# Kernel tuning notes

Hardware: AMD Instinct MI355X
Metric: run time of the kernel (lower is better)

Reference implementation:

```python
import jax, jax.numpy as jnp
import numpy as np
import math

B, NQ, NK = 8, 1024, 2048
DQ = DK = DV = 1024
H = 8
DH = DV // H
EPS = 1e-5


def _layernorm(x, g, b):
    mu = jnp.mean(x, axis=-1, keepdims=True)
    var = jnp.mean(jnp.square(x - mu), axis=-1, keepdims=True)
    return (x - mu) * jax.lax.rsqrt(var + EPS) * g + b


def setup_inputs() -> dict:
    key = jax.random.key(0)
    ks = jax.random.split(key, 12)
    s_q = 1.0 / math.sqrt(DQ)
    s_v = 1.0 / math.sqrt(DV)
    return {
        "Q": jax.random.normal(ks[0], (B, NQ, DQ), jnp.float32),
        "K": jax.random.normal(ks[1], (B, NK, DK), jnp.float32),
        "Wq": jax.random.normal(ks[2], (DQ, DV), jnp.float32) * s_q,
        "bq": jnp.zeros((DV,), jnp.float32),
        "Wk": jax.random.normal(ks[3], (DK, DV), jnp.float32) * s_q,
        "bk": jnp.zeros((DV,), jnp.float32),
        "Wv": jax.random.normal(ks[4], (DK, DV), jnp.float32) * s_q,
        "bv": jnp.zeros((DV,), jnp.float32),
        "Wo": jax.random.normal(ks[5], (DV, DV), jnp.float32) * s_v,
        "bo": jnp.zeros((DV,), jnp.float32),
        "g0": jnp.ones((DV,), jnp.float32),
        "b0": jnp.zeros((DV,), jnp.float32),
        "g1": jnp.ones((DV,), jnp.float32),
        "b1": jnp.zeros((DV,), jnp.float32),
    }


def reference(Q, K, Wq, bq, Wk, bk, Wv, bv, Wo, bo, g0, b0, g1, b1):
    # projections
    q = Q @ Wq + bq                      # [B, NQ, DV]
    k = K @ Wk + bk                      # [B, NK, DV]
    v = K @ Wv + bv                      # [B, NK, DV]
    qh = q.reshape(B, NQ, H, DH)
    kh = k.reshape(B, NK, H, DH)
    vh = v.reshape(B, NK, H, DH)
    # NOTE: original scales by sqrt(dim_V), not sqrt(d_head)
    scale = 1.0 / math.sqrt(DV)
    logits = jnp.einsum("bqhd,bkhd->bhqk", qh, kh) * scale
    A = jax.nn.softmax(logits, axis=-1)
    # residual baked into attention output: Q_ + A @ V_
    Oh = qh + jnp.einsum("bhqk,bkhd->bqhd", A, vh)
    O = Oh.reshape(B, NQ, DV)
    O = _layernorm(O, g0, b0)
    O = O + jax.nn.relu(O @ Wo + bo)
    O = _layernorm(O, g1, b1)
    return O
```

## Files before the change

kernel.cpp:

```cpp
#include <hip/hip_runtime.h>
#include <stdint.h>

#define DEVI static __device__ __forceinline__

typedef __attribute__((ext_vector_type(8))) short short8;
typedef __attribute__((ext_vector_type(4))) float floatx4;
typedef __attribute__((ext_vector_type(4))) unsigned short ushortx4;

DEVI unsigned short f2bf(float f) {
  union { float f; uint32_t u; } v; v.f = f;
  uint32_t r = v.u + 0x7FFFu + ((v.u >> 16) & 1u);
  return (unsigned short)(r >> 16);
}
DEVI unsigned short f2bf_trunc(float f) {
  union { float f; uint32_t u; } v; v.f = f;
  return (unsigned short)(v.u >> 16);
}
DEVI float bf2f(unsigned short s) {
  union { uint32_t u; float f; } v; v.u = ((uint32_t)s) << 16;
  return v.f;
}
DEVI uint32_t fbits(float f) {
  union { float f; uint32_t u; } v; v.f = f;
  return v.u;
}
DEVI unsigned char f2fp8(float f) {
  return (unsigned char)(__builtin_amdgcn_cvt_pk_fp8_f32(f, f, 0, false) & 0xff);
}

DEVI void lds_cp16(void* lds, const void* g) {
  __builtin_amdgcn_global_load_lds(
      (const __attribute__((address_space(1))) uint32_t*)g,
      reinterpret_cast<__attribute__((address_space(3))) uint32_t*>(
          (uint32_t)reinterpret_cast<uintptr_t>(lds)),
      16, 0, 0);
}

__global__ __launch_bounds__(256) void cvt_qk(const float* __restrict__ Q,
                                              const float* __restrict__ K,
                                              unsigned short* __restrict__ Qb,
                                              unsigned char* __restrict__ Kf8) {
  const int bid = blockIdx.x;
  if (bid < 8192) {
    const size_t i = (size_t)bid * 256 + threadIdx.x;
    const floatx4 v = ((const floatx4*)Q)[i];
    ushortx4 o;
    o.x = f2bf(v.x); o.y = f2bf(v.y); o.z = f2bf(v.z); o.w = f2bf(v.w);
    ((ushortx4*)Qb)[i] = o;
  } else {
    const size_t i = (size_t)(bid - 8192) * 256 + threadIdx.x;
    const floatx4 v = ((const floatx4*)K)[i];
    int p = __builtin_amdgcn_cvt_pk_fp8_f32(v.x, v.y, 0, false);
    p = __builtin_amdgcn_cvt_pk_fp8_f32(v.z, v.w, p, true);
    ((int*)Kf8)[i] = p;
  }
}

__global__ __launch_bounds__(256) void wtrans4(const float* __restrict__ Wq,
                                               const float* __restrict__ Wk,
                                               const float* __restrict__ Wv,
                                               const float* __restrict__ Wo,
                                               unsigned short* __restrict__ Wt,
                                               unsigned char* __restrict__ Wt8) {
  __shared__ float t[32][33];
  const int tx = threadIdx.x, ty = threadIdx.y;
  const int z = blockIdx.z;
  const float* W = (z == 0) ? Wq : (z == 1) ? Wk : (z == 2) ? Wv : Wo;
  const int c0 = blockIdx.x * 32, r0 = blockIdx.y * 32;
#pragma unroll
  for (int i = 0; i < 4; i++)
    t[ty + i * 8][tx] = W[(size_t)(r0 + ty + i * 8) * 1024 + c0 + tx];
  __syncthreads();
  if (z == 0 || z == 3) {
    unsigned short* D = Wt + (z == 0 ? 0 : (size_t)1024 * 1024);
#pragma unroll
    for (int i = 0; i < 4; i++)
      D[(size_t)(c0 + ty + i * 8) * 1024 + r0 + tx] = f2bf(t[tx][ty + i * 8]);
  } else {
    unsigned char* D = Wt8 + (z == 1 ? 0 : (size_t)1024 * 1024);
#pragma unroll
    for (int i = 0; i < 4; i++)
      D[(size_t)(c0 + ty + i * 8) * 1024 + r0 + tx] = f2fp8(t[tx][ty + i * 8]);
  }
}

template <int EPI>
__global__ __launch_bounds__(256, 3) void gemm_bt(
    const unsigned short* __restrict__ A, const unsigned short* __restrict__ Bt,
    const float* __restrict__ bias, const unsigned short* __restrict__ X1,
    void* __restrict__ Cout) {
  __shared__ unsigned short As[2][4][128][8];
  __shared__ unsigned short Bs[2][4][128][8];

  const int tid = threadIdx.x;
  const int lane = tid & 63, w = tid >> 6;
  const int wr = w >> 1, wc = w & 1;
  const int qd = lane >> 4, l16 = lane & 15;
  const int bid = blockIdx.x;
  const int xcd = bid & 7, loc = bid >> 3;
  const int m0 = (xcd * 8 + (loc & 7)) * 128;
  const int n0 = (loc >> 3) * 128;

  floatx4 acc[4][4];
#pragma unroll
  for (int i = 0; i < 4; i++)
#pragma unroll
    for (int j = 0; j < 4; j++) { floatx4 z = {0.f, 0.f, 0.f, 0.f}; acc[i][j] = z; }

  const int prow = tid & 127;
  const unsigned short* aptr = A + (size_t)(m0 + prow) * 1024 + ((tid >> 7) << 3);
  const unsigned short* bptr = Bt + (size_t)(n0 + prow) * 1024 + ((tid >> 7) << 3);
  const int dstoff = tid * 8;

  lds_cp16(&As[0][0][0][0] + dstoff, aptr);
  lds_cp16(&As[0][0][0][0] + dstoff + 2048, aptr + 16);
  lds_cp16(&Bs[0][0][0][0] + dstoff, bptr);
  lds_cp16(&Bs[0][0][0][0] + dstoff + 2048, bptr + 16);

  for (int it = 0; it < 32; it++) {
    __syncthreads();
    if (it < 31) {
      const int nb = (it + 1) & 1, k0 = (it + 1) * 32;
      lds_cp16(&As[nb][0][0][0] + dstoff, aptr + k0);
      lds_cp16(&As[nb][0][0][0] + dstoff + 2048, aptr + k0 + 16);
      lds_cp16(&Bs[nb][0][0][0] + dstoff, bptr + k0);
      lds_cp16(&Bs[nb][0][0][0] + dstoff + 2048, bptr + k0 + 16);
    }
    const int cur = it & 1;
    short8 af[4], bf[4];
#pragma unroll
    for (int mi = 0; mi < 4; mi++)
      af[mi] = *(const short8*)&As[cur][qd][wr * 64 + mi * 16 + l16][0];
#pragma unroll
    for (int ni = 0; ni < 4; ni++)
      bf[ni] = *(const short8*)&Bs[cur][qd][wc * 64 + ni * 16 + l16][0];
#pragma unroll
    for (int mi = 0; mi < 4; mi++)
#pragma unroll
      for (int ni = 0; ni < 4; ni++)
        acc[mi][ni] =
            __builtin_amdgcn_mfma_f32_16x16x32_bf16(af[mi], bf[ni], acc[mi][ni], 0, 0, 0);
  }

#pragma unroll
  for (int mi = 0; mi < 4; mi++) {
#pragma unroll
    for (int ni = 0; ni < 4; ni++) {
      const int row = m0 + wr * 64 + mi * 16 + qd * 4;
      const int col = n0 + wc * 64 + ni * 16 + l16;
      const float bv = bias[col];
      if constexpr (EPI == 0) {
        unsigned short* C = (unsigned short*)Cout;
#pragma unroll
        for (int r = 0; r < 4; r++)
          C[(size_t)(row + r) * 1024 + col] = f2bf(acc[mi][ni][r] + bv);
      } else {
        float* C = (float*)Cout;
#pragma unroll
        for (int r = 0; r < 4; r++) {
          const float x1 = bf2f(X1[(size_t)(row + r) * 1024 + col]);
          C[(size_t)(row + r) * 1024 + col] = x1 + fmaxf(acc[mi][ni][r] + bv, 0.f);
        }
      }
    }
  }
}

__global__ __launch_bounds__(256, 3) void gemm_kv_f8(
    const unsigned char* __restrict__ A, const unsigned char* __restrict__ Bt,
    const float* __restrict__ biasK, const float* __restrict__ biasV,
    unsigned short* __restrict__ CK, unsigned char* __restrict__ CV8) {
  __shared__ unsigned char As[2][4][128][16];
  __shared__ unsigned char Bs[2][4][128][16];

  const int tid = threadIdx.x;
  const int lane = tid & 63, w = tid >> 6;
  const int wr = w >> 1, wc = w & 1;
  const int qd = lane >> 4, l16 = lane & 15;
  const int bid = blockIdx.x;
  const int xcd = bid & 7, loc = bid >> 3;
  const int m0 = (xcd * 16 + (loc & 15)) * 128;
  const int n0 = (loc >> 4) * 128;

  floatx4 acc[4][4];
#pragma unroll
  for (int i = 0; i < 4; i++)
#pragma unroll
    for (int j = 0; j < 4; j++) { floatx4 z = {0.f, 0.f, 0.f, 0.f}; acc[i][j] = z; }

  const int srow = tid & 127, sc = tid >> 7;
  const unsigned char* aptr = A + (size_t)(m0 + srow) * 1024 + sc * 16;
  const unsigned char* bptr = Bt + (size_t)(n0 + srow) * 1024 + sc * 16;
  unsigned char* dA = &As[0][sc][srow][0];
  unsigned char* dB = &Bs[0][sc][srow][0];

  lds_cp16(dA, aptr);
  lds_cp16(dA + 4096, aptr + 32);
  lds_cp16(dB, bptr);
  lds_cp16(dB + 4096, bptr + 32);

  for (int it = 0; it < 16; it++) {
    __syncthreads();
    if (it < 15) {
      const int nb = (it + 1) & 1, k0 = (it + 1) * 64;
      lds_cp16(dA + nb * 8192, aptr + k0);
      lds_cp16(dA + nb * 8192 + 4096, aptr + k0 + 32);
      lds_cp16(dB + nb * 8192, bptr + k0);
      lds_cp16(dB + nb * 8192 + 4096, bptr + k0 + 32);
    }
    const int cur = it & 1;
    const int coff = (qd & 1) * 8, chi = qd >> 1;
    long a8[4][2], b8[4][2];
#pragma unroll
    for (int mi = 0; mi < 4; mi++) {
      const int row = wr * 64 + mi * 16 + l16;
      a8[mi][0] = *(const long*)&As[cur][chi][row][coff];
      a8[mi][1] = *(const long*)&As[cur][2 + chi][row][coff];
    }
#pragma unroll
    for (int ni = 0; ni < 4; ni++) {
      const int row = wc * 64 + ni * 16 + l16;
      b8[ni][0] = *(const long*)&Bs[cur][chi][row][coff];
      b8[ni][1] = *(const long*)&Bs[cur][2 + chi][row][coff];
    }
#pragma unroll
    for (int mi = 0; mi < 4; mi++)
#pragma unroll
      for (int ni = 0; ni < 4; ni++)
        acc[mi][ni] = __builtin_amdgcn_mfma_f32_16x16x32_fp8_fp8(
            a8[mi][0], b8[ni][0], acc[mi][ni], 0, 0, 0);
#pragma unroll
    for (int mi = 0; mi < 4; mi++)
#pragma unroll
      for (int ni = 0; ni < 4; ni++)
        acc[mi][ni] = __builtin_amdgcn_mfma_f32_16x16x32_fp8_fp8(
            a8[mi][1], b8[ni][1], acc[mi][ni], 0, 0, 0);
  }

#pragma unroll
  for (int mi = 0; mi < 4; mi++) {
#pragma unroll
    for (int ni = 0; ni < 4; ni++) {
      const int row = m0 + wr * 64 + mi * 16 + qd * 4;
      const int col = n0 + wc * 64 + ni * 16 + l16;
      if (col < 1024) {
        const float bv = biasK[col];
#pragma unroll
        for (int r = 0; r < 4; r++)
          CK[(size_t)(row + r) * 1024 + col] = f2bf(acc[mi][ni][r] + bv);
      } else {
        const int vc = col - 1024;
        const float bv = biasV[vc];
        const int bb = row >> 11, nk = row & 2047;
        const int hh = vc >> 7, dh = vc & 127;
        int p = __builtin_amdgcn_cvt_pk_fp8_f32(acc[mi][ni][0] + bv,
                                                acc[mi][ni][1] + bv, 0, false);
        p = __builtin_amdgcn_cvt_pk_fp8_f32(acc[mi][ni][2] + bv,
                                            acc[mi][ni][3] + bv, p, true);
        *(uint32_t*)&CV8[((((size_t)(bb * 8 + hh)) * 256 + (nk >> 3)) * 128 + dh) * 8 +
                         (nk & 7)] = (uint32_t)p;
      }
    }
  }
}

__global__ __launch_bounds__(256, 3) void attn(
    const unsigned short* __restrict__ qb, const unsigned short* __restrict__ kb,
    const unsigned char* __restrict__ vt8, unsigned short* __restrict__ Ob) {
  __shared__ __align__(16) unsigned char smc[32768];
  unsigned short* sm16 = (unsigned short*)smc;

  const int tid = threadIdx.x;
  const int lane = tid & 63, w = tid >> 6;
  const int qd = lane >> 4, l16 = lane & 15;
  const int bid = blockIdx.x;
  const int qt = bid >> 6, bh = bid & 63;
  const int h = bh >> 3, b = bh & 7;
  const int m0 = qt * 128;

  const size_t qbase = ((size_t)(b * 1024 + m0)) * 1024 + h * 128;
  const size_t kbase = ((size_t)(b * 2048)) * 1024 + h * 128;
  const size_t vbase8 = (size_t)(b * 8 + h) * 262144;

#pragma unroll
  for (int i = 0; i < 8; i++) {
    const int p = i * 256 + tid;
    const int row = p & 127, c = p >> 7;
    lds_cp16(&sm16[c * 1024 + row * 8], qb + qbase + (size_t)row * 1024 + c * 8);
  }
  __syncthreads();
  short8 qf[2][4];
#pragma unroll
  for (int nt = 0; nt < 2; nt++)
#pragma unroll
    for (int ks = 0; ks < 4; ks++)
      qf[nt][ks] =
          *(const short8*)&sm16[(ks * 4 + qd) * 1024 + (w * 32 + nt * 16 + l16) * 8];
  __syncthreads();

#pragma unroll
  for (int i = 0; i < 2; i++) {
    const int p = i * 256 + tid;
    const int kr = p & 31, kc = p >> 5;
    lds_cp16(smc + kc * 512 + kr * 16, kb + kbase + (size_t)kr * 1024 + kc * 8);
  }
  {
    const int vc = tid >> 6, d2 = (tid & 63) * 2;
    lds_cp16(smc + 16384 + vc * 1024 + d2 * 8, vt8 + vbase8 + vc * 1024 + d2 * 8);
  }

  floatx4 oacc[8][2];
#pragma unroll
  for (int mt = 0; mt < 8; mt++)
#pragma unroll
    for (int nt = 0; nt < 2; nt++) { floatx4 z = {0.f, 0.f, 0.f, 0.f}; oacc[mt][nt] = z; }
  float lsum[2] = {0.f, 0.f};

  const int addrLo = ((qd & 1) * 32 + l16) * 4;
  const int addrHi = addrLo + 64;
  const bool loHalf = (lane < 32);

  for (int it = 0; it < 64; it++) {
    __syncthreads();
    if (it + 1 < 64) {
      const int nb = (it + 1) & 1, kv0 = (it + 1) * 32;
#pragma unroll
      for (int i = 0; i < 2; i++) {
        const int p = i * 256 + tid;
        const int kr = p & 31, kc = p >> 5;
        lds_cp16(smc + nb * 8192 + kc * 512 + kr * 16,
                 kb + kbase + (size_t)(kv0 + kr) * 1024 + kc * 8);
      }
      {
        const int vc = tid >> 6, d2 = (tid & 63) * 2;
        lds_cp16(smc + 16384 + nb * 4096 + vc * 1024 + d2 * 8,
                 vt8 + vbase8 + (size_t)kv0 * 128 + vc * 1024 + d2 * 8);
      }
    }
    const int cur = it & 1;

    floatx4 st[2][2];
#pragma unroll
    for (int mt = 0; mt < 2; mt++)
#pragma unroll
      for (int nt = 0; nt < 2; nt++) { floatx4 z = {0.f, 0.f, 0.f, 0.f}; st[mt][nt] = z; }
    __builtin_amdgcn_s_setprio(1);
#pragma unroll
    for (int ks = 0; ks < 4; ks++) {
      const short8 ka =
          *(const short8*)(smc + cur * 8192 + (ks * 4 + qd) * 512 + l16 * 16);
      const short8 kb2 =
          *(const short8*)(smc + cur * 8192 + (ks * 4 + qd) * 512 + (16 + l16) * 16);
#pragma unroll
      for (int nt = 0; nt < 2; nt++) {
        st[0][nt] = __builtin_amdgcn_mfma_f32_16x16x32_bf16(ka, qf[nt][ks], st[0][nt], 0, 0, 0);
        st[1][nt] = __builtin_amdgcn_mfma_f32_16x16x32_bf16(kb2, qf[nt][ks], st[1][nt], 0, 0, 0);
      }
    }
    __builtin_amdgcn_s_setprio(0);

    long vl[8];
#pragma unroll
    for (int mt = 0; mt < 8; mt++)
      vl[mt] = *(const long*)(smc + 16384 + cur * 4096 + qd * 1024 + (mt * 16 + l16) * 8);

    uint32_t pkf[2][2];
#pragma unroll
    for (int mt = 0; mt < 2; mt++)
#pragma unroll
      for (int nt = 0; nt < 2; nt++) {
        const float e0 = __expf(st[mt][nt][0] * 0.03125f);
        const float e1 = __expf(st[mt][nt][1] * 0.03125f);
        const float e2 = __expf(st[mt][nt][2] * 0.03125f);
        const float e3 = __expf(st[mt][nt][3] * 0.03125f);
        lsum[nt] += (e0 + e1) + (e2 + e3);
        int p = __builtin_amdgcn_cvt_pk_fp8_f32(e0, e1, 0, false);
        p = __builtin_amdgcn_cvt_pk_fp8_f32(e2, e3, p, true);
        pkf[mt][nt] = (uint32_t)p;
      }

#pragma unroll
    for (int nt = 0; nt < 2; nt++) {
      int lo0 = __builtin_amdgcn_ds_bpermute(addrLo, (int)pkf[0][nt]);
      int lo1 = __builtin_amdgcn_ds_bpermute(addrLo, (int)pkf[1][nt]);
      int hi0 = __builtin_amdgcn_ds_bpermute(addrHi, (int)pkf[0][nt]);
      int hi1 = __builtin_amdgcn_ds_bpermute(addrHi, (int)pkf[1][nt]);
      union { int i[2]; long l; } u;
      u.i[0] = loHalf ? lo0 : lo1;
      u.i[1] = loHalf ? hi0 : hi1;
      const long pfl = u.l;
      __builtin_amdgcn_s_setprio(1);
#pragma unroll
      for (int mt = 0; mt < 8; mt++)
        oacc[mt][nt] =
            __builtin_amdgcn_mfma_f32_16x16x32_fp8_fp8(vl[mt], pfl, oacc[mt][nt], 0, 0, 0);
      __builtin_amdgcn_s_setprio(0);
    }
  }

  float inv[2];
#pragma unroll
  for (int nt = 0; nt < 2; nt++) {
    float s = lsum[nt];
    s += __shfl_xor(s, 16);
    s += __shfl_xor(s, 32);
    inv[nt] = 1.f / s;
  }

  __syncthreads();
#pragma unroll
  for (int mt = 0; mt < 8; mt++)
#pragma unroll
    for (int nt = 0; nt < 2; nt++) {
      const int q = w * 32 + nt * 16 + l16;
#pragma unroll
      for (int r = 0; r < 4; r++) {
        const int dh = mt * 16 + qd * 4 + r;
        const int c = dh >> 3, off = dh & 7;
        sm16[q * 128 + ((c ^ (q & 15)) * 8) + off] = f2bf_trunc(oacc[mt][nt][r] * inv[nt]);
      }
    }
  __syncthreads();
#pragma unroll
  for (int i = 0; i < 8; i++) {
    const int p = i * 256 + tid;
    const int row = p >> 4, c = p & 15;
    const short8 ov = *(const short8*)&sm16[row * 128 + ((c ^ (row & 15)) * 8)];
    const short8 qres = *(const short8*)(qb + qbase + (size_t)row * 1024 + c * 8);
    union { unsigned short us[8]; short8 s; } o;
#pragma unroll
    for (int e = 0; e < 8; e++)
      o.us[e] = f2bf(bf2f((unsigned short)ov[e]) + bf2f((unsigned short)qres[e]));
    *(short8*)(Ob + qbase + (size_t)row * 1024 + c * 8) = o.s;
  }
}

__global__ __launch_bounds__(256) void ln_rows(const unsigned short* __restrict__ X,
                                               const float* __restrict__ g,
                                               const float* __restrict__ bb,
                                               unsigned short* __restrict__ Y) {
  __shared__ float red[8];
  const int row = blockIdx.x, tid = threadIdx.x;
  const int w = tid >> 6, lane = tid & 63;
  const ushortx4 u = ((const ushortx4*)(X + (size_t)row * 1024))[tid];
  float x0 = bf2f(u.x), x1 = bf2f(u.y), x2 = bf2f(u.z), x3 = bf2f(u.w);
  float s = x0 + x1 + x2 + x3;
  float s2 = x0 * x0 + x1 * x1 + x2 * x2 + x3 * x3;
#pragma unroll
  for (int off = 1; off < 64; off <<= 1) { s += __shfl_xor(s, off); s2 += __shfl_xor(s2, off); }
  if (lane == 0) { red[w] = s; red[4 + w] = s2; }
  __syncthreads();
  s = red[0] + red[1] + red[2] + red[3];
  s2 = red[4] + red[5] + red[6] + red[7];
  const float mu = s * (1.f / 1024.f);
  const float rs = rsqrtf(s2 * (1.f / 1024.f) - mu * mu + 1e-5f);
  const floatx4 gv = ((const floatx4*)g)[tid];
  const floatx4 bv = ((const floatx4*)bb)[tid];
  ushortx4 o;
  o.x = f2bf((x0 - mu) * rs * gv.x + bv.x);
  o.y = f2bf((x1 - mu) * rs * gv.y + bv.y);
  o.z = f2bf((x2 - mu) * rs * gv.z + bv.z);
  o.w = f2bf((x3 - mu) * rs * gv.w + bv.w);
  ((ushortx4*)(Y + (size_t)row * 1024))[tid] = o;
}

__global__ __launch_bounds__(256) void ln_f32(const float* __restrict__ X,
                                              const float* __restrict__ g,
                                              const float* __restrict__ bb,
                                              float* __restrict__ out) {
  __shared__ float red[8];
  const int row = blockIdx.x, tid = threadIdx.x;
  const int w = tid >> 6, lane = tid & 63;
  const floatx4 xv = ((const floatx4*)(X + (size_t)row * 1024))[tid];
  float x0 = xv.x, x1 = xv.y, x2 = xv.z, x3 = xv.w;
  float s = x0 + x1 + x2 + x3;
  float s2 = x0 * x0 + x1 * x1 + x2 * x2 + x3 * x3;
#pragma unroll
  for (int off = 1; off < 64; off <<= 1) { s += __shfl_xor(s, off); s2 += __shfl_xor(s2, off); }
  if (lane == 0) { red[w] = s; red[4 + w] = s2; }
  __syncthreads();
  s = red[0] + red[1] + red[2] + red[3];
  s2 = red[4] + red[5] + red[6] + red[7];
  const float mu = s * (1.f / 1024.f);
  const float rs = rsqrtf(s2 * (1.f / 1024.f) - mu * mu + 1e-5f);
  const floatx4 gv = ((const floatx4*)g)[tid];
  const floatx4 bv = ((const floatx4*)bb)[tid];
  floatx4 o;
  o.x = (x0 - mu) * rs * gv.x + bv.x;
  o.y = (x1 - mu) * rs * gv.y + bv.y;
  o.z = (x2 - mu) * rs * gv.z + bv.z;
  o.w = (x3 - mu) * rs * gv.w + bv.w;
  ((floatx4*)(out + (size_t)row * 1024))[tid] = o;
}

extern "C" void kernel_launch(void* const* d_in, const int* in_sizes, int n_in,
                              void* d_out, int out_size, void* d_ws, size_t ws_size,
                              hipStream_t stream) {
  (void)in_sizes; (void)n_in; (void)out_size; (void)ws_size;
  const float* Q  = (const float*)d_in[0];
  const float* K  = (const float*)d_in[1];
  const float* Wq = (const float*)d_in[2];
  const float* bq = (const float*)d_in[3];
  const float* Wk = (const float*)d_in[4];
  const float* bk = (const float*)d_in[5];
  const float* Wv = (const float*)d_in[6];
  const float* bv = (const float*)d_in[7];
  const float* Wo = (const float*)d_in[8];
  const float* bo = (const float*)d_in[9];
  const float* g0 = (const float*)d_in[10];
  const float* b0 = (const float*)d_in[11];
  const float* g1 = (const float*)d_in[12];
  const float* b1 = (const float*)d_in[13];
  float* out = (float*)d_out;

  char* ws = (char*)d_ws;
  const size_t MB = 1u << 20;
  unsigned short* Qb  = (unsigned short*)(ws + 0);
  unsigned short* X1  = (unsigned short*)(ws + 16 * MB);
  unsigned short* Wt  = (unsigned short*)(ws + 32 * MB);
  unsigned char*  Wt8 = (unsigned char*)(ws + 36 * MB);
  unsigned char*  Kf8 = (unsigned char*)(ws + 38 * MB);
  unsigned short* qbp = (unsigned short*)(ws + 54 * MB);
  unsigned short* kbp = (unsigned short*)(ws + 70 * MB);
  unsigned char*  vt8 = (unsigned char*)(ws + 102 * MB);
  unsigned short* O   = Qb;
  float* O2 = (float*)(ws + 70 * MB);

  unsigned short* Wqt = Wt;
  unsigned short* Wot = Wt + (size_t)1024 * 1024;

  cvt_qk<<<24576, 256, 0, stream>>>(Q, K, Qb, Kf8);
  wtrans4<<<dim3(32, 32, 4), dim3(32, 8), 0, stream>>>(Wq, Wk, Wv, Wo, Wt, Wt8);

  gemm_bt<0><<<512, 256, 0, stream>>>(Qb, Wqt, bq, nullptr, qbp);
  gemm_kv_f8<<<2048, 256, 0, stream>>>(Kf8, Wt8, bk, bv, kbp, vt8);
  attn<<<512, 256, 0, stream>>>(qbp, kbp, vt8, O);
  ln_rows<<<8192, 256, 0, stream>>>(O, g0, b0, X1);
  gemm_bt<2><<<512, 256, 0, stream>>>(X1, Wot, bo, X1, O2);
  ln_f32<<<8192, 256, 0, stream>>>(O2, g1, b1, out);
}
```

Before: 412.9 us.

## Deepen KV fp8 GEMM pipeline to four stages and store pre-LN output in bf16

The K/V fp8 projection GEMM moves from double buffering to a four-buffer LDS ring. Three stages are prefetched and explicit vmcnt waits plus raw barriers replace __syncthreads, and the fragment loads become 16-byte vector reads. Occupancy is lowered to 2 blocks per CU to fit the larger LDS footprint. Separately, the Wo GEMM epilogue now writes the residual+ReLU result as bf16 instead of fp32, and the final layernorm reads bf16. This halves that intermediate's traffic at the cost of extra rounding before the last normalization.

```diff
diff --git a/kernel.cpp b/kernel.cpp
--- a/kernel.cpp
+++ b/kernel.cpp
@@ -6,6 +6,7 @@
 typedef __attribute__((ext_vector_type(8))) short short8;
 typedef __attribute__((ext_vector_type(4))) float floatx4;
 typedef __attribute__((ext_vector_type(4))) unsigned short ushortx4;
+typedef __attribute__((ext_vector_type(2))) long longx2;
 
 DEVI unsigned short f2bf(float f) {
   union { float f; uint32_t u; } v; v.f = f;
@@ -155,23 +156,23 @@
         for (int r = 0; r < 4; r++)
           C[(size_t)(row + r) * 1024 + col] = f2bf(acc[mi][ni][r] + bv);
       } else {
-        float* C = (float*)Cout;
+        unsigned short* C = (unsigned short*)Cout;
 #pragma unroll
         for (int r = 0; r < 4; r++) {
           const float x1 = bf2f(X1[(size_t)(row + r) * 1024 + col]);
-          C[(size_t)(row + r) * 1024 + col] = x1 + fmaxf(acc[mi][ni][r] + bv, 0.f);
+          C[(size_t)(row + r) * 1024 + col] = f2bf(x1 + fmaxf(acc[mi][ni][r] + bv, 0.f));
         }
       }
     }
   }
 }
 
-__global__ __launch_bounds__(256, 3) void gemm_kv_f8(
+__global__ __launch_bounds__(256, 2) void gemm_kv_f8(
     const unsigned char* __restrict__ A, const unsigned char* __restrict__ Bt,
     const float* __restrict__ biasK, const float* __restrict__ biasV,
     unsigned short* __restrict__ CK, unsigned char* __restrict__ CV8) {
-  __shared__ unsigned char As[2][4][128][16];
-  __shared__ unsigned char Bs[2][4][128][16];
+  __shared__ unsigned char As[4][4][128][16];
+  __shared__ unsigned char Bs[4][4][128][16];
 
   const int tid = threadIdx.x;
   const int lane = tid & 63, w = tid >> 6;
@@ -191,51 +192,60 @@
   const int srow = tid & 127, sc = tid >> 7;
   const unsigned char* aptr = A + (size_t)(m0 + srow) * 1024 + sc * 16;
   const unsigned char* bptr = Bt + (size_t)(n0 + srow) * 1024 + sc * 16;
-  unsigned char* dA = &As[0][sc][srow][0];
-  unsigned char* dB = &Bs[0][sc][srow][0];
-
-  lds_cp16(dA, aptr);
-  lds_cp16(dA + 4096, aptr + 32);
-  lds_cp16(dB, bptr);
-  lds_cp16(dB + 4096, bptr + 32);
+  unsigned char* dA0 = &As[0][sc][srow][0];
+  unsigned char* dB0 = &Bs[0][sc][srow][0];
+
+#define KV_STAGE(step)                                   \
+  {                                                      \
+    const int buf_ = (step) & 3, k0_ = (step) * 64;      \
+    lds_cp16(dA0 + buf_ * 8192, aptr + k0_);             \
+    lds_cp16(dA0 + buf_ * 8192 + 4096, aptr + k0_ + 32); \
+    lds_cp16(dB0 + buf_ * 8192, bptr + k0_);             \
+    lds_cp16(dB0 + buf_ * 8192 + 4096, bptr + k0_ + 32); \
+  }
+
+  KV_STAGE(0);
+  KV_STAGE(1);
+  KV_STAGE(2);
 
   for (int it = 0; it < 16; it++) {
-    __syncthreads();
-    if (it < 15) {
-      const int nb = (it + 1) & 1, k0 = (it + 1) * 64;
-      lds_cp16(dA + nb * 8192, aptr + k0);
-      lds_cp16(dA + nb * 8192 + 4096, aptr + k0 + 32);
-      lds_cp16(dB + nb * 8192, bptr + k0);
-      lds_cp16(dB + nb * 8192 + 4096, bptr + k0 + 32);
-    }
-    const int cur = it & 1;
-    const int coff = (qd & 1) * 8, chi = qd >> 1;
-    long a8[4][2], b8[4][2];
+    if (it < 13) KV_STAGE(it + 3);
+    if (it < 13)       asm volatile("s_waitcnt vmcnt(12)" ::: "memory");
+    else if (it == 13) asm volatile("s_waitcnt vmcnt(8)" ::: "memory");
+    else if (it == 14) asm volatile("s_waitcnt vmcnt(4)" ::: "memory");
+    else               asm volatile("s_waitcnt vmcnt(0)" ::: "memory");
+    __builtin_amdgcn_s_barrier();
+    __builtin_amdgcn_sched_barrier(0);
+
+    const int cur = it & 3;
+    longx2 av[4], bvv[4];
 #pragma unroll
     for (int mi = 0; mi < 4; mi++) {
       const int row = wr * 64 + mi * 16 + l16;
-      a8[mi][0] = *(const long*)&As[cur][chi][row][coff];
-      a8[mi][1] = *(const long*)&As[cur][2 + chi][row][coff];
+      av[mi] = *(const longx2*)&As[cur][qd][row][0];
     }
 #pragma unroll
     for (int ni = 0; ni < 4; ni++) {
       const int row = wc * 64 + ni * 16 + l16;
-      b8[ni][0] = *(const long*)&Bs[cur][chi][row][coff];
-      b8[ni][1] = *(const long*)&Bs[cur][2 + chi][row][coff];
+      bvv[ni] = *(const longx2*)&Bs[cur][qd][row][0];
     }
 #pragma unroll
     for (int mi = 0; mi < 4; mi++)
 #pragma unroll
       for (int ni = 0; ni < 4; ni++)
         acc[mi][ni] = __builtin_amdgcn_mfma_f32_16x16x32_fp8_fp8(
-            a8[mi][0], b8[ni][0], acc[mi][ni], 0, 0, 0);
+            av[mi].x, bvv[ni].x, acc[mi][ni], 0, 0, 0);
 #pragma unroll
     for (int mi = 0; mi < 4; mi++)
 #pragma unroll
       for (int ni = 0; ni < 4; ni++)
         acc[mi][ni] = __builtin_amdgcn_mfma_f32_16x16x32_fp8_fp8(
-            a8[mi][1], b8[ni][1], acc[mi][ni], 0, 0, 0);
-  }
+            av[mi].y, bvv[ni].y, acc[mi][ni], 0, 0, 0);
+
+    __builtin_amdgcn_sched_barrier(0);
+    __builtin_amdgcn_s_barrier();
+  }
+#undef KV_STAGE
 
 #pragma unroll
   for (int mi = 0; mi < 4; mi++) {
@@ -464,15 +474,15 @@
   ((ushortx4*)(Y + (size_t)row * 1024))[tid] = o;
 }
 
-__global__ __launch_bounds__(256) void ln_f32(const float* __restrict__ X,
+__global__ __launch_bounds__(256) void ln_b2f(const unsigned short* __restrict__ X,
                                               const float* __restrict__ g,
                                               const float* __restrict__ bb,
                                               float* __restrict__ out) {
   __shared__ float red[8];
   const int row = blockIdx.x, tid = threadIdx.x;
   const int w = tid >> 6, lane = tid & 63;
-  const floatx4 xv = ((const floatx4*)(X + (size_t)row * 1024))[tid];
-  float x0 = xv.x, x1 = xv.y, x2 = xv.z, x3 = xv.w;
+  const ushortx4 u = ((const ushortx4*)(X + (size_t)row * 1024))[tid];
+  float x0 = bf2f(u.x), x1 = bf2f(u.y), x2 = bf2f(u.z), x3 = bf2f(u.w);
   float s = x0 + x1 + x2 + x3;
   float s2 = x0 * x0 + x1 * x1 + x2 * x2 + x3 * x3;
 #pragma unroll
@@ -524,7 +534,7 @@
   unsigned short* kbp = (unsigned short*)(ws + 70 * MB);
   unsigned char*  vt8 = (unsigned char*)(ws + 102 * MB);
   unsigned short* O   = Qb;
-  float* O2 = (float*)(ws + 70 * MB);
+  unsigned short* O2b = (unsigned short*)(ws + 70 * MB);
 
   unsigned short* Wqt = Wt;
   unsigned short* Wot = Wt + (size_t)1024 * 1024;
@@ -536,6 +546,6 @@
   gemm_kv_f8<<<2048, 256, 0, stream>>>(Kf8, Wt8, bk, bv, kbp, vt8);
   attn<<<512, 256, 0, stream>>>(qbp, kbp, vt8, O);
   ln_rows<<<8192, 256, 0, stream>>>(O, g0, b0, X1);
-  gemm_bt<2><<<512, 256, 0, stream>>>(X1, Wot, bo, X1, O2);
-  ln_f32<<<8192, 256, 0, stream>>>(O2, g1, b1, out);
-}
+  gemm_bt<2><<<512, 256, 0, stream>>>(X1, Wot, bo, X1, O2b);
+  ln_b2f<<<8192, 256, 0, stream>>>(O2b, g1, b1, out);
+}
```

Measured after the change: 419.2 us. No clear change (+1.5%).

## Store K projection in fp8 and run QK^T with fp8 MFMA; bf16 pre-LN output

Applied to the files above, without the earlier changes.

The K projection is now written as fp8, and the attention kernel converts Q fragments to fp8 so it can compute logits with fp8 MFMA. K tiles are staged in LDS using an XOR-swizzled layout, which halves K traffic and shared memory per tile. The KV GEMM now reads its LDS fragments with one 16-byte load instead of two 8-byte loads. The output GEMM writes a bf16 intermediate instead of fp32, and the final layernorm reads bf16. These changes cut memory traffic and raise MFMA throughput, at the cost of lower precision in the logits and the residual.

```diff
diff --git a/kernel.cpp b/kernel.cpp
--- a/kernel.cpp
+++ b/kernel.cpp
@@ -6,6 +6,7 @@
 typedef __attribute__((ext_vector_type(8))) short short8;
 typedef __attribute__((ext_vector_type(4))) float floatx4;
 typedef __attribute__((ext_vector_type(4))) unsigned short ushortx4;
+typedef __attribute__((ext_vector_type(2))) long longx2;
 
 DEVI unsigned short f2bf(float f) {
   union { float f; uint32_t u; } v; v.f = f;
@@ -26,6 +27,19 @@
 }
 DEVI unsigned char f2fp8(float f) {
   return (unsigned char)(__builtin_amdgcn_cvt_pk_fp8_f32(f, f, 0, false) & 0xff);
+}
+DEVI long pack8fp8(const short8 s) {
+  int a = __builtin_amdgcn_cvt_pk_fp8_f32(bf2f((unsigned short)s[0]),
+                                          bf2f((unsigned short)s[1]), 0, false);
+  a = __builtin_amdgcn_cvt_pk_fp8_f32(bf2f((unsigned short)s[2]),
+                                      bf2f((unsigned short)s[3]), a, true);
+  int b = __builtin_amdgcn_cvt_pk_fp8_f32(bf2f((unsigned short)s[4]),
+                                          bf2f((unsigned short)s[5]), 0, false);
+  b = __builtin_amdgcn_cvt_pk_fp8_f32(bf2f((unsigned short)s[6]),
+                                      bf2f((unsigned short)s[7]), b, true);
+  union { int i[2]; long l; } u;
+  u.i[0] = a; u.i[1] = b;
+  return u.l;
 }
 
 DEVI void lds_cp16(void* lds, const void* g) {
@@ -155,11 +169,11 @@
         for (int r = 0; r < 4; r++)
           C[(size_t)(row + r) * 1024 + col] = f2bf(acc[mi][ni][r] + bv);
       } else {
-        float* C = (float*)Cout;
+        unsigned short* C = (unsigned short*)Cout;
 #pragma unroll
         for (int r = 0; r < 4; r++) {
           const float x1 = bf2f(X1[(size_t)(row + r) * 1024 + col]);
-          C[(size_t)(row + r) * 1024 + col] = x1 + fmaxf(acc[mi][ni][r] + bv, 0.f);
+          C[(size_t)(row + r) * 1024 + col] = f2bf(x1 + fmaxf(acc[mi][ni][r] + bv, 0.f));
         }
       }
     }
@@ -169,7 +183,7 @@
 __global__ __launch_bounds__(256, 3) void gemm_kv_f8(
     const unsigned char* __restrict__ A, const unsigned char* __restrict__ Bt,
     const float* __restrict__ biasK, const float* __restrict__ biasV,
-    unsigned short* __restrict__ CK, unsigned char* __restrict__ CV8) {
+    unsigned char* __restrict__ CK8, unsigned char* __restrict__ CV8) {
   __shared__ unsigned char As[2][4][128][16];
   __shared__ unsigned char Bs[2][4][128][16];
 
@@ -209,32 +223,29 @@
       lds_cp16(dB + nb * 8192 + 4096, bptr + k0 + 32);
     }
     const int cur = it & 1;
-    const int coff = (qd & 1) * 8, chi = qd >> 1;
-    long a8[4][2], b8[4][2];
+    longx2 av[4], bvv[4];
 #pragma unroll
     for (int mi = 0; mi < 4; mi++) {
       const int row = wr * 64 + mi * 16 + l16;
-      a8[mi][0] = *(const long*)&As[cur][chi][row][coff];
-      a8[mi][1] = *(const long*)&As[cur][2 + chi][row][coff];
+      av[mi] = *(const longx2*)&As[cur][qd][row][0];
     }
 #pragma unroll
     for (int ni = 0; ni < 4; ni++) {
       const int row = wc * 64 + ni * 16 + l16;
-      b8[ni][0] = *(const long*)&Bs[cur][chi][row][coff];
-      b8[ni][1] = *(const long*)&Bs[cur][2 + chi][row][coff];
+      bvv[ni] = *(const longx2*)&Bs[cur][qd][row][0];
     }
 #pragma unroll
     for (int mi = 0; mi < 4; mi++)
 #pragma unroll
       for (int ni = 0; ni < 4; ni++)
         acc[mi][ni] = __builtin_amdgcn_mfma_f32_16x16x32_fp8_fp8(
-            a8[mi][0], b8[ni][0], acc[mi][ni], 0, 0, 0);
+            av[mi].x, bvv[ni].x, acc[mi][ni], 0, 0, 0);
 #pragma unroll
     for (int mi = 0; mi < 4; mi++)
 #pragma unroll
       for (int ni = 0; ni < 4; ni++)
         acc[mi][ni] = __builtin_amdgcn_mfma_f32_16x16x32_fp8_fp8(
-            a8[mi][1], b8[ni][1], acc[mi][ni], 0, 0, 0);
+            av[mi].y, bvv[ni].y, acc[mi][ni], 0, 0, 0);
   }
 
 #pragma unroll
@@ -247,7 +258,7 @@
         const float bv = biasK[col];
 #pragma unroll
         for (int r = 0; r < 4; r++)
-          CK[(size_t)(row + r) * 1024 + col] = f2bf(acc[mi][ni][r] + bv);
+          CK8[(size_t)(row + r) * 1024 + col] = f2fp8(acc[mi][ni][r] + bv);
       } else {
         const int vc = col - 1024;
         const float bv = biasV[vc];
@@ -265,7 +276,7 @@
 }
 
 __global__ __launch_bounds__(256, 3) void attn(
-    const unsigned short* __restrict__ qb, const unsigned short* __restrict__ kb,
+    const unsigned short* __restrict__ qb, const unsigned char* __restrict__ kb8,
     const unsigned char* __restrict__ vt8, unsigned short* __restrict__ Ob) {
   __shared__ __align__(16) unsigned char smc[32768];
   unsigned short* sm16 = (unsigned short*)smc;
@@ -279,7 +290,7 @@
   const int m0 = qt * 128;
 
   const size_t qbase = ((size_t)(b * 1024 + m0)) * 1024 + h * 128;
-  const size_t kbase = ((size_t)(b * 2048)) * 1024 + h * 128;
+  const size_t kbase8 = ((size_t)(b * 2048)) * 1024 + h * 128;
   const size_t vbase8 = (size_t)(b * 8 + h) * 262144;
 
 #pragma unroll
@@ -289,24 +300,25 @@
     lds_cp16(&sm16[c * 1024 + row * 8], qb + qbase + (size_t)row * 1024 + c * 8);
   }
   __syncthreads();
-  short8 qf[2][4];
-#pragma unroll
-  for (int nt = 0; nt < 2; nt++)
-#pragma unroll
-    for (int ks = 0; ks < 4; ks++)
-      qf[nt][ks] =
-          *(const short8*)&sm16[(ks * 4 + qd) * 1024 + (w * 32 + nt * 16 + l16) * 8];
-  __syncthreads();
-
-#pragma unroll
-  for (int i = 0; i < 2; i++) {
-    const int p = i * 256 + tid;
-    const int kr = p & 31, kc = p >> 5;
-    lds_cp16(smc + kc * 512 + kr * 16, kb + kbase + (size_t)kr * 1024 + kc * 8);
-  }
+  long qx[2][2], qy[2][2];
+#pragma unroll
+  for (int p = 0; p < 2; p++)
+#pragma unroll
+    for (int nt = 0; nt < 2; nt++) {
+      const int row = w * 32 + nt * 16 + l16;
+      const short8 qa = *(const short8*)&sm16[(p * 8 + qd * 2) * 1024 + row * 8];
+      const short8 qc = *(const short8*)&sm16[(p * 8 + qd * 2 + 1) * 1024 + row * 8];
+      qx[p][nt] = pack8fp8(qa);
+      qy[p][nt] = pack8fp8(qc);
+    }
+  __syncthreads();
+
   {
-    const int vc = tid >> 6, d2 = (tid & 63) * 2;
-    lds_cp16(smc + 16384 + vc * 1024 + d2 * 8, vt8 + vbase8 + vc * 1024 + d2 * 8);
+    const int kr = tid >> 3, sl = tid & 7;
+    lds_cp16(smc + tid * 16,
+             kb8 + kbase8 + (size_t)kr * 1024 + (sl ^ (kr & 7)) * 16);
+    lds_cp16(smc + 8192 + tid * 16,
+             vt8 + vbase8 + (size_t)(tid >> 6) * 1024 + (tid & 63) * 16);
   }
 
   floatx4 oacc[8][2];
@@ -324,18 +336,11 @@
     __syncthreads();
     if (it + 1 < 64) {
       const int nb = (it + 1) & 1, kv0 = (it + 1) * 32;
-#pragma unroll
-      for (int i = 0; i < 2; i++) {
-        const int p = i * 256 + tid;
-        const int kr = p & 31, kc = p >> 5;
-        lds_cp16(smc + nb * 8192 + kc * 512 + kr * 16,
-                 kb + kbase + (size_t)(kv0 + kr) * 1024 + kc * 8);
-      }
-      {
-        const int vc = tid >> 6, d2 = (tid & 63) * 2;
-        lds_cp16(smc + 16384 + nb * 4096 + vc * 1024 + d2 * 8,
-                 vt8 + vbase8 + (size_t)kv0 * 128 + vc * 1024 + d2 * 8);
-      }
+      const int kr = tid >> 3, sl = tid & 7;
+      lds_cp16(smc + nb * 4096 + tid * 16,
+               kb8 + kbase8 + (size_t)(kv0 + kr) * 1024 + (sl ^ (kr & 7)) * 16);
+      lds_cp16(smc + 8192 + nb * 4096 + tid * 16,
+               vt8 + vbase8 + (size_t)kv0 * 128 + (tid >> 6) * 1024 + (tid & 63) * 16);
     }
     const int cur = it & 1;
 
@@ -346,15 +351,15 @@
       for (int nt = 0; nt < 2; nt++) { floatx4 z = {0.f, 0.f, 0.f, 0.f}; st[mt][nt] = z; }
     __builtin_amdgcn_s_setprio(1);
 #pragma unroll
-    for (int ks = 0; ks < 4; ks++) {
-      const short8 ka =
-          *(const short8*)(smc + cur * 8192 + (ks * 4 + qd) * 512 + l16 * 16);
-      const short8 kb2 =
-          *(const short8*)(smc + cur * 8192 + (ks * 4 + qd) * 512 + (16 + l16) * 16);
-#pragma unroll
-      for (int nt = 0; nt < 2; nt++) {
-        st[0][nt] = __builtin_amdgcn_mfma_f32_16x16x32_bf16(ka, qf[nt][ks], st[0][nt], 0, 0, 0);
-        st[1][nt] = __builtin_amdgcn_mfma_f32_16x16x32_bf16(kb2, qf[nt][ks], st[1][nt], 0, 0, 0);
+    for (int p = 0; p < 2; p++) {
+#pragma unroll
+      for (int mt = 0; mt < 2; mt++) {
+        const longx2 kk = *(const longx2*)(smc + cur * 4096 + (mt * 16 + l16) * 128 +
+                                           (((p * 4 + qd) ^ (l16 & 7)) << 4));
+        st[mt][0] = __builtin_amdgcn_mfma_f32_16x16x32_fp8_fp8(kk.x, qx[p][0], st[mt][0], 0, 0, 0);
+        st[mt][1] = __builtin_amdgcn_mfma_f32_16x16x32_fp8_fp8(kk.x, qx[p][1], st[mt][1], 0, 0, 0);
+        st[mt][0] = __builtin_amdgcn_mfma_f32_16x16x32_fp8_fp8(kk.y, qy[p][0], st[mt][0], 0, 0, 0);
+        st[mt][1] = __builtin_amdgcn_mfma_f32_16x16x32_fp8_fp8(kk.y, qy[p][1], st[mt][1], 0, 0, 0);
       }
     }
     __builtin_amdgcn_s_setprio(0);
@@ -362,7 +367,7 @@
     long vl[8];
 #pragma unroll
     for (int mt = 0; mt < 8; mt++)
-      vl[mt] = *(const long*)(smc + 16384 + cur * 4096 + qd * 1024 + (mt * 16 + l16) * 8);
+      vl[mt] = *(const long*)(smc + 8192 + cur * 4096 + qd * 1024 + (mt * 16 + l16) * 8);
 
     uint32_t pkf[2][2];
 #pragma unroll
@@ -464,15 +469,15 @@
   ((ushortx4*)(Y + (size_t)row * 1024))[tid] = o;
 }
 
-__global__ __launch_bounds__(256) void ln_f32(const float* __restrict__ X,
+__global__ __launch_bounds__(256) void ln_b2f(const unsigned short* __restrict__ X,
                                               const float* __restrict__ g,
                                               const float* __restrict__ bb,
                                               float* __restrict__ out) {
   __shared__ float red[8];
   const int row = blockIdx.x, tid = threadIdx.x;
   const int w = tid >> 6, lane = tid & 63;
-  const floatx4 xv = ((const floatx4*)(X + (size_t)row * 1024))[tid];
-  float x0 = xv.x, x1 = xv.y, x2 = xv.z, x3 = xv.w;
+  const ushortx4 u = ((const ushortx4*)(X + (size_t)row * 1024))[tid];
+  float x0 = bf2f(u.x), x1 = bf2f(u.y), x2 = bf2f(u.z), x3 = bf2f(u.w);
   float s = x0 + x1 + x2 + x3;
   float s2 = x0 * x0 + x1 * x1 + x2 * x2 + x3 * x3;
 #pragma unroll
@@ -521,10 +526,10 @@
   unsigned char*  Wt8 = (unsigned char*)(ws + 36 * MB);
   unsigned char*  Kf8 = (unsigned char*)(ws + 38 * MB);
   unsigned short* qbp = (unsigned short*)(ws + 54 * MB);
-  unsigned short* kbp = (unsigned short*)(ws + 70 * MB);
+  unsigned char*  kb8p = (unsigned char*)(ws + 70 * MB);
   unsigned char*  vt8 = (unsigned char*)(ws + 102 * MB);
   unsigned short* O   = Qb;
-  float* O2 = (float*)(ws + 70 * MB);
+  unsigned short* O2b = (unsigned short*)(ws + 70 * MB);
 
   unsigned short* Wqt = Wt;
   unsigned short* Wot = Wt + (size_t)1024 * 1024;
@@ -533,9 +538,9 @@
   wtrans4<<<dim3(32, 32, 4), dim3(32, 8), 0, stream>>>(Wq, Wk, Wv, Wo, Wt, Wt8);
 
   gemm_bt<0><<<512, 256, 0, stream>>>(Qb, Wqt, bq, nullptr, qbp);
-  gemm_kv_f8<<<2048, 256, 0, stream>>>(Kf8, Wt8, bk, bv, kbp, vt8);
-  attn<<<512, 256, 0, stream>>>(qbp, kbp, vt8, O);
+  gemm_kv_f8<<<2048, 256, 0, stream>>>(Kf8, Wt8, bk, bv, kb8p, vt8);
+  attn<<<512, 256, 0, stream>>>(qbp, kb8p, vt8, O);
   ln_rows<<<8192, 256, 0, stream>>>(O, g0, b0, X1);
-  gemm_bt<2><<<512, 256, 0, stream>>>(X1, Wot, bo, X1, O2);
-  ln_f32<<<8192, 256, 0, stream>>>(O2, g1, b1, out);
-}
+  gemm_bt<2><<<512, 256, 0, stream>>>(X1, Wot, bo, X1, O2b);
+  ln_b2f<<<8192, 256, 0, stream>>>(O2b, g1, b1, out);
+}
```

Result: no change. 407.9 us (-1.2%).
